# Optimization experiments

Hardware: AMD Instinct MI355X
Metric: run time of the kernel (lower is better)

Reference implementation:

```python
import jax, jax.numpy as jnp
import numpy as np

B, S, D, H = 2, 2048, 1024, 16
HD = D // H           # head_dim = 64
WINDOW = 64           # sparse_block_size (default attention_window)
GLOBAL = 16           # global_tokens


def setup_inputs() -> dict:
    key = jax.random.key(0)
    ks = jax.random.split(key, 12)
    sc = 0.02
    return {
        "query": jax.random.normal(ks[0], (B, S, D), jnp.float32),
        "key":   jax.random.normal(ks[1], (B, S, D), jnp.float32),
        "value": jax.random.normal(ks[2], (B, S, D), jnp.float32),
        "Wq": jax.random.normal(ks[3], (D, D), jnp.float32) * sc,
        "bq": jnp.zeros((D,), jnp.float32),
        "Wk": jax.random.normal(ks[4], (D, D), jnp.float32) * sc,
        "bk": jnp.zeros((D,), jnp.float32),
        "Wv": jax.random.normal(ks[5], (D, D), jnp.float32) * sc,
        "bv": jnp.zeros((D,), jnp.float32),
        "Wo": jax.random.normal(ks[6], (D, D), jnp.float32) * sc,
        "bo": jnp.zeros((D,), jnp.float32),
    }


def _sparse_mask(seq_len, window, n_global):
    # band: j in [i - window//2, i + window//2] inclusive
    idx = jnp.arange(seq_len)
    band = jnp.abs(idx[:, None] - idx[None, :]) <= (window // 2)
    glob = (idx[:, None] < n_global) | (idx[None, :] < n_global)
    return (band | glob)  # [S, S] bool


def reference(query, key, value, Wq, bq, Wk, bk, Wv, bv, Wo, bo):
    # projections (torch Linear: x @ W.T + b), split heads -> [B, H, S, HD]
    def heads(x, W, b):
        return (x @ W.T + b).reshape(B, -1, H, HD).transpose(0, 2, 1, 3)

    q = heads(query, Wq, bq)
    k = heads(key, Wk, bk)
    v = heads(value, Wv, bv)

    scores = jnp.einsum("bhqd,bhkd->bhqk", q, k) / jnp.sqrt(jnp.float32(HD))
    mask = _sparse_mask(S, WINDOW, GLOBAL)  # [S, S]
    scores = jnp.where(mask[None, None, :, :], scores, jnp.float32(-1e9))
    attn = jax.nn.softmax(scores, axis=-1)  # dropout is identity in eval
    ctx = jnp.einsum("bhqk,bhkd->bhqd", attn, v)
    out = ctx.transpose(0, 2, 1, 3).reshape(B, -1, D) @ Wo.T + bo
    return out, attn
```

## Files before the change

kernel.cpp:

```cpp
#include <hip/hip_runtime.h>
#include <hip/hip_bf16.h>
#include <hip/hip_fp16.h>

typedef _Float16 half8 __attribute__((ext_vector_type(8)));
typedef _Float16 half4 __attribute__((ext_vector_type(4)));
typedef float f32x4 __attribute__((ext_vector_type(4)));

#define S_LEN 2048
#define D_MODEL 1024
#define NH 16
#define HEAD_D 64
#define BATCH 2
#define NGLOB 16

__global__ __launch_bounds__(256) void cvt_f32_f16(const float* __restrict__ src,
                                                   _Float16* __restrict__ dst, int n) {
  int i = (blockIdx.x * 256 + threadIdx.x) * 4;
  if (i < n) {
    f32x4 v = *(const f32x4*)(src + i);
    half4 h;
    h[0] = (_Float16)v[0]; h[1] = (_Float16)v[1];
    h[2] = (_Float16)v[2]; h[3] = (_Float16)v[3];
    *(half4*)(dst + i) = h;
  }
}

__device__ __forceinline__ void load_lds16(const void* g, void* l) {
  __builtin_amdgcn_global_load_lds((const __attribute__((address_space(1))) void*)g,
                                   (__attribute__((address_space(3))) void*)l, 16, 0, 0);
}

__global__ __launch_bounds__(256) void gemm_bt_f16(
    const _Float16* __restrict__ A,
    const _Float16* __restrict__ W,
    const float*    __restrict__ bias,
    float*          __restrict__ Cf,
    _Float16*       __restrict__ Ch,
    int M, int N, int K)
{
  __shared__ _Float16 sA[128 * 32];
  __shared__ _Float16 sW[128 * 32];
  const int tid = threadIdx.x;
  const int l = tid & 63;
  const int w = tid >> 6;
  const int wr = w >> 1, wc = w & 1;
  const int m0 = blockIdx.y * 128, n0 = blockIdx.x * 128;

  f32x4 acc[4][4] = {};

  for (int k0 = 0; k0 < K; k0 += 32) {
    {
      int c = tid;
      int row = c >> 2, kc = c & 3;
      load_lds16(A + (size_t)(m0 + row) * K + k0 + kc * 8, sA + c * 8);
      load_lds16(W + (size_t)(n0 + row) * K + k0 + kc * 8, sW + c * 8);
      c = tid + 256;
      row = c >> 2; kc = c & 3;
      load_lds16(A + (size_t)(m0 + row) * K + k0 + kc * 8, sA + c * 8);
      load_lds16(W + (size_t)(n0 + row) * K + k0 + kc * 8, sW + c * 8);
    }
    __syncthreads();

    half8 av[4], bv[4];
#pragma unroll
    for (int mi = 0; mi < 4; ++mi)
      av[mi] = *(const half8*)&sA[(wr * 64 + mi * 16 + (l & 15)) * 32 + (l >> 4) * 8];
#pragma unroll
    for (int ni = 0; ni < 4; ++ni)
      bv[ni] = *(const half8*)&sW[(wc * 64 + ni * 16 + (l & 15)) * 32 + (l >> 4) * 8];
#pragma unroll
    for (int mi = 0; mi < 4; ++mi)
#pragma unroll
      for (int ni = 0; ni < 4; ++ni)
        acc[mi][ni] = __builtin_amdgcn_mfma_f32_16x16x32_f16(av[mi], bv[ni], acc[mi][ni], 0, 0, 0);
    __syncthreads();
  }

#pragma unroll
  for (int mi = 0; mi < 4; ++mi) {
#pragma unroll
    for (int ni = 0; ni < 4; ++ni) {
      int row = m0 + wr * 64 + mi * 16 + ((l >> 4) << 2);
      int col = n0 + wc * 64 + ni * 16 + (l & 15);
      float bc = bias[col];
#pragma unroll
      for (int r = 0; r < 4; ++r) {
        float v = acc[mi][ni][r] + bc;
        size_t idx = (size_t)(row + r) * N + col;
        if (Cf) Cf[idx] = v;
        if (Ch) Ch[idx] = (_Float16)v;
      }
    }
  }
}

__global__ __launch_bounds__(256) void attn_band(
    const _Float16* __restrict__ Qh, const _Float16* __restrict__ Kh,
    const _Float16* __restrict__ Vh,
    float* __restrict__ attn, _Float16* __restrict__ ctx)
{
  __shared__ float Kb[96 * 65];
  __shared__ float Vb[96 * 65];
  __shared__ float Kg[16 * 65];
  __shared__ float Vg[16 * 65];
  __shared__ float qbuf[4][64];
  __shared__ float pbuf[4][128];

  const int bid = blockIdx.x;
  const int rb = bid & 63;
  const int h  = (bid >> 6) & 15;
  const int b  = bid >> 10;
  const int i0 = rb * 32;
  const int jb0 = max(i0 - 32, 0);
  const int jb1 = min(i0 + 63, S_LEN - 1);
  const int Wn = jb1 - jb0 + 1;
  const int tid = threadIdx.x;

  for (int s = tid; s < Wn * 16; s += 256) {
    int j = s >> 4, d4 = (s & 15) << 2;
    size_t base = ((size_t)b * S_LEN + jb0 + j) * D_MODEL + h * HEAD_D + d4;
    half4 kv = *(const half4*)(Kh + base);
    half4 vv = *(const half4*)(Vh + base);
    int o = j * 65 + d4;
    Kb[o] = (float)kv[0]; Kb[o+1] = (float)kv[1]; Kb[o+2] = (float)kv[2]; Kb[o+3] = (float)kv[3];
    Vb[o] = (float)vv[0]; Vb[o+1] = (float)vv[1]; Vb[o+2] = (float)vv[2]; Vb[o+3] = (float)vv[3];
  }
  {
    int s = tid;
    int j = s >> 4, d4 = (s & 15) << 2;
    size_t base = ((size_t)b * S_LEN + j) * D_MODEL + h * HEAD_D + d4;
    half4 kv = *(const half4*)(Kh + base);
    half4 vv = *(const half4*)(Vh + base);
    int o = j * 65 + d4;
    Kg[o] = (float)kv[0]; Kg[o+1] = (float)kv[1]; Kg[o+2] = (float)kv[2]; Kg[o+3] = (float)kv[3];
    Vg[o] = (float)vv[0]; Vg[o+1] = (float)vv[1]; Vg[o+2] = (float)vv[2]; Vg[o+3] = (float)vv[3];
  }
  __syncthreads();

  const int l = tid & 63, w = tid >> 6;
  for (int rr = 0; rr < 8; ++rr) {
    const int i = i0 + w * 8 + rr;
    if (i < NGLOB) continue;

    qbuf[w][l] = (float)Qh[((size_t)b * S_LEN + i) * D_MODEL + h * HEAD_D + l];

    const int b0n = max(i - 32, 16);
    const int b1n = min(i + 32, S_LEN - 1);
    const int nj = 16 + (b1n - b0n + 1);

    const int  j1 = (l < 16) ? l : (b0n + l - 16);
    const bool v1 = l < nj;
    const int  jj2 = l + 64;
    const bool v2 = jj2 < nj;
    const int  j2 = v2 ? (b0n + jj2 - 16) : b0n;

    const float* kr1 = (l < 16) ? &Kg[l * 65] : &Kb[((v1 ? j1 : b0n) - jb0) * 65];
    const float* kr2 = &Kb[(j2 - jb0) * 65];

    float s1 = 0.f, s2 = 0.f;
#pragma unroll 8
    for (int d = 0; d < 64; ++d) {
      float qd = qbuf[w][d];
      s1 += qd * kr1[d];
      s2 += qd * kr2[d];
    }
    s1 *= 0.125f; s2 *= 0.125f;
    if (!v1) s1 = -1e30f;
    if (!v2) s2 = -1e30f;

    float mx = fmaxf(s1, s2);
#pragma unroll
    for (int o = 32; o; o >>= 1) mx = fmaxf(mx, __shfl_xor(mx, o));
    float e1 = v1 ? __expf(s1 - mx) : 0.f;
    float e2 = v2 ? __expf(s2 - mx) : 0.f;
    float sm = e1 + e2;
#pragma unroll
    for (int o = 32; o; o >>= 1) sm += __shfl_xor(sm, o);
    float inv = 1.f / sm;
    float p1 = e1 * inv, p2 = e2 * inv;

    pbuf[w][l] = p1;
    pbuf[w][64 + l] = p2;

    float* arow = attn + ((size_t)(b * NH + h) * S_LEN + i) * S_LEN;
#pragma unroll
    for (int t = 0; t < 8; ++t) {
      const int lo = t * 256;
      const int j0 = lo + l * 4;
      f32x4 o4 = {0.f, 0.f, 0.f, 0.f};
      const bool hasAny = (lo < NGLOB) || !((b1n < lo) || (b0n >= lo + 256));
      if (hasAny) {
#pragma unroll
        for (int r = 0; r < 4; ++r) {
          int j = j0 + r;
          float v = 0.f;
          if (j < NGLOB) v = pbuf[w][j];
          else if (j >= b0n && j <= b1n) v = pbuf[w][16 + j - b0n];
          o4[r] = v;
        }
      }
      *(f32x4*)(arow + j0) = o4;
    }

    float c = 0.f;
    for (int jj = 0; jj < nj; ++jj) {
      float p = pbuf[w][jj];
      const float* vr = (jj < 16) ? &Vg[jj * 65] : &Vb[(b0n + jj - 16 - jb0) * 65];
      c += p * vr[l];
    }
    ctx[((size_t)b * S_LEN + i) * D_MODEL + h * HEAD_D + l] = (_Float16)c;
  }
}

__global__ __launch_bounds__(256) void attn_global(
    const _Float16* __restrict__ Qh, const _Float16* __restrict__ Kh,
    const _Float16* __restrict__ Vh,
    float* __restrict__ attn, _Float16* __restrict__ ctx)
{
  __shared__ float p[S_LEN];
  __shared__ float qbuf[64];
  __shared__ float red[8];
  __shared__ float part[4][64];

  const int bid = blockIdx.x;
  const int i = bid & 15;
  const int h = (bid >> 4) & 15;
  const int b = bid >> 8;
  const int tid = threadIdx.x;

  if (tid < 64) qbuf[tid] = (float)Qh[((size_t)b * S_LEN + i) * D_MODEL + h * HEAD_D + tid];
  __syncthreads();

  float lmax = -1e30f;
  for (int j = tid; j < S_LEN; j += 256) {
    const half8* kr = (const half8*)(Kh + ((size_t)b * S_LEN + j) * D_MODEL + h * HEAD_D);
    float s = 0.f;
#pragma unroll
    for (int c8 = 0; c8 < 8; ++c8) {
      half8 kv = kr[c8];
#pragma unroll
      for (int r = 0; r < 8; ++r) s += qbuf[c8 * 8 + r] * (float)kv[r];
    }
    s *= 0.125f;
    p[j] = s;
    lmax = fmaxf(lmax, s);
  }
#pragma unroll
  for (int o = 32; o; o >>= 1) lmax = fmaxf(lmax, __shfl_xor(lmax, o));
  if ((tid & 63) == 0) red[tid >> 6] = lmax;
  __syncthreads();
  const float mx = fmaxf(fmaxf(red[0], red[1]), fmaxf(red[2], red[3]));

  float lsum = 0.f;
  for (int j = tid; j < S_LEN; j += 256) {
    float e = __expf(p[j] - mx);
    p[j] = e;
    lsum += e;
  }
#pragma unroll
  for (int o = 32; o; o >>= 1) lsum += __shfl_xor(lsum, o);
  if ((tid & 63) == 0) red[4 + (tid >> 6)] = lsum;
  __syncthreads();
  const float inv = 1.f / (red[4] + red[5] + red[6] + red[7]);

  float* arow = attn + ((size_t)(b * NH + h) * S_LEN + i) * S_LEN;
  for (int j = tid; j < S_LEN; j += 256) {
    float pv = p[j] * inv;
    p[j] = pv;
    arow[j] = pv;
  }
  __syncthreads();

  const int d = tid & 63, c4 = tid >> 6;
  float c = 0.f;
  for (int j = c4 * 512; j < c4 * 512 + 512; ++j)
    c += p[j] * (float)Vh[((size_t)b * S_LEN + j) * D_MODEL + h * HEAD_D + d];
  part[c4][d] = c;
  __syncthreads();
  if (tid < 64) {
    float cc = part[0][tid] + part[1][tid] + part[2][tid] + part[3][tid];
    ctx[((size_t)b * S_LEN + i) * D_MODEL + h * HEAD_D + tid] = (_Float16)cc;
  }
}

extern "C" void kernel_launch(void* const* d_in, const int* in_sizes, int n_in,
                              void* d_out, int out_size, void* d_ws, size_t ws_size,
                              hipStream_t stream) {
  const float* query = (const float*)d_in[0];
  const float* key   = (const float*)d_in[1];
  const float* value = (const float*)d_in[2];
  const float* Wq = (const float*)d_in[3];
  const float* bq = (const float*)d_in[4];
  const float* Wk = (const float*)d_in[5];
  const float* bk = (const float*)d_in[6];
  const float* Wv = (const float*)d_in[7];
  const float* bv = (const float*)d_in[8];
  const float* Wo = (const float*)d_in[9];
  const float* bo = (const float*)d_in[10];

  float* out  = (float*)d_out;
  float* attn = out + (size_t)BATCH * S_LEN * D_MODEL;

  const size_t XN = (size_t)BATCH * S_LEN * D_MODEL;
  const size_t WN = (size_t)D_MODEL * D_MODEL;
  _Float16* ws   = (_Float16*)d_ws;
  _Float16* X16  = ws;
  _Float16* W16q = ws + XN;
  _Float16* W16k = W16q + WN;
  _Float16* W16v = W16k + WN;
  _Float16* W16o = W16v + WN;
  _Float16* Q16  = W16o + WN;
  _Float16* K16  = Q16 + XN;
  _Float16* V16  = K16 + XN;
  _Float16* C16  = V16 + XN;

  const int M = BATCH * S_LEN;

  cvt_f32_f16<<<WN / 1024, 256, 0, stream>>>(Wq, W16q, (int)WN);
  cvt_f32_f16<<<WN / 1024, 256, 0, stream>>>(Wk, W16k, (int)WN);
  cvt_f32_f16<<<WN / 1024, 256, 0, stream>>>(Wv, W16v, (int)WN);
  cvt_f32_f16<<<WN / 1024, 256, 0, stream>>>(Wo, W16o, (int)WN);

  dim3 gg(D_MODEL / 128, M / 128);

  cvt_f32_f16<<<XN / 1024, 256, 0, stream>>>(query, X16, (int)XN);
  gemm_bt_f16<<<gg, 256, 0, stream>>>(X16, W16q, bq, nullptr, Q16, M, D_MODEL, D_MODEL);
  cvt_f32_f16<<<XN / 1024, 256, 0, stream>>>(key, X16, (int)XN);
  gemm_bt_f16<<<gg, 256, 0, stream>>>(X16, W16k, bk, nullptr, K16, M, D_MODEL, D_MODEL);
  cvt_f32_f16<<<XN / 1024, 256, 0, stream>>>(value, X16, (int)XN);
  gemm_bt_f16<<<gg, 256, 0, stream>>>(X16, W16v, bv, nullptr, V16, M, D_MODEL, D_MODEL);

  attn_band<<<BATCH * NH * (S_LEN / 32), 256, 0, stream>>>(Q16, K16, V16, attn, C16);
  attn_global<<<BATCH * NH * NGLOB, 256, 0, stream>>>(Q16, K16, V16, attn, C16);

  gemm_bt_f16<<<gg, 256, 0, stream>>>(C16, W16o, bo, out, nullptr, M, D_MODEL, D_MODEL);
}
```

Baseline: 845.5 us.

## Batch QKV projections and conversions into single launches, narrow output GEMM tiles

Merges the three input conversions and four weight conversions into two grid-indexed kernels, and runs the Q/K/V projections as one GEMM launch with a z-dimension selecting the operand set. The output projection now uses a 128x64 tile kernel, which doubles the block count from 256 to 512 and fills more CUs on a 256-CU device. The aim is to cut launch overhead and raise occupancy for the GEMMs. It needs two extra fp16 activation buffers in the workspace, because the inputs no longer share one buffer.

Result: faster. 789.4 us (-6.6%).

```diff
diff --git a/kernel.cpp b/kernel.cpp
--- a/kernel.cpp
+++ b/kernel.cpp
@@ -13,15 +13,35 @@
 #define BATCH 2
 #define NGLOB 16
 
-__global__ __launch_bounds__(256) void cvt_f32_f16(const float* __restrict__ src,
-                                                   _Float16* __restrict__ dst, int n) {
+__global__ __launch_bounds__(256) void cvt_in3(
+    const float* __restrict__ s0, const float* __restrict__ s1, const float* __restrict__ s2,
+    _Float16* __restrict__ d0, _Float16* __restrict__ d1, _Float16* __restrict__ d2, int n) {
+  const float* s = (blockIdx.y == 0) ? s0 : (blockIdx.y == 1) ? s1 : s2;
+  _Float16*   d = (blockIdx.y == 0) ? d0 : (blockIdx.y == 1) ? d1 : d2;
   int i = (blockIdx.x * 256 + threadIdx.x) * 4;
   if (i < n) {
-    f32x4 v = *(const f32x4*)(src + i);
+    f32x4 v = *(const f32x4*)(s + i);
     half4 h;
     h[0] = (_Float16)v[0]; h[1] = (_Float16)v[1];
     h[2] = (_Float16)v[2]; h[3] = (_Float16)v[3];
-    *(half4*)(dst + i) = h;
+    *(half4*)(d + i) = h;
+  }
+}
+
+__global__ __launch_bounds__(256) void cvt_w4(
+    const float* __restrict__ s0, const float* __restrict__ s1,
+    const float* __restrict__ s2, const float* __restrict__ s3,
+    _Float16* __restrict__ d0, _Float16* __restrict__ d1,
+    _Float16* __restrict__ d2, _Float16* __restrict__ d3, int n) {
+  const float* s = (blockIdx.y == 0) ? s0 : (blockIdx.y == 1) ? s1 : (blockIdx.y == 2) ? s2 : s3;
+  _Float16*   d = (blockIdx.y == 0) ? d0 : (blockIdx.y == 1) ? d1 : (blockIdx.y == 2) ? d2 : d3;
+  int i = (blockIdx.x * 256 + threadIdx.x) * 4;
+  if (i < n) {
+    f32x4 v = *(const f32x4*)(s + i);
+    half4 h;
+    h[0] = (_Float16)v[0]; h[1] = (_Float16)v[1];
+    h[2] = (_Float16)v[2]; h[3] = (_Float16)v[3];
+    *(half4*)(d + i) = h;
   }
 }
 
@@ -30,14 +50,19 @@
                                    (__attribute__((address_space(3))) void*)l, 16, 0, 0);
 }
 
-__global__ __launch_bounds__(256) void gemm_bt_f16(
-    const _Float16* __restrict__ A,
-    const _Float16* __restrict__ W,
-    const float*    __restrict__ bias,
-    float*          __restrict__ Cf,
-    _Float16*       __restrict__ Ch,
+__global__ __launch_bounds__(256) void gemm_qkv_f16(
+    const _Float16* __restrict__ A0, const _Float16* __restrict__ A1, const _Float16* __restrict__ A2,
+    const _Float16* __restrict__ W0, const _Float16* __restrict__ W1, const _Float16* __restrict__ W2,
+    const float* __restrict__ b0, const float* __restrict__ b1, const float* __restrict__ b2,
+    _Float16* __restrict__ C0, _Float16* __restrict__ C1, _Float16* __restrict__ C2,
     int M, int N, int K)
 {
+  const int z = blockIdx.z;
+  const _Float16* A = (z == 0) ? A0 : (z == 1) ? A1 : A2;
+  const _Float16* W = (z == 0) ? W0 : (z == 1) ? W1 : W2;
+  const float* bias = (z == 0) ? b0 : (z == 1) ? b1 : b2;
+  _Float16* Ch      = (z == 0) ? C0 : (z == 1) ? C1 : C2;
+
   __shared__ _Float16 sA[128 * 32];
   __shared__ _Float16 sW[128 * 32];
   const int tid = threadIdx.x;
@@ -86,10 +111,66 @@
 #pragma unroll
       for (int r = 0; r < 4; ++r) {
         float v = acc[mi][ni][r] + bc;
-        size_t idx = (size_t)(row + r) * N + col;
-        if (Cf) Cf[idx] = v;
-        if (Ch) Ch[idx] = (_Float16)v;
+        Ch[(size_t)(row + r) * N + col] = (_Float16)v;
       }
+    }
+  }
+}
+
+__global__ __launch_bounds__(256) void gemm_bt64_f16(
+    const _Float16* __restrict__ A,
+    const _Float16* __restrict__ W,
+    const float*    __restrict__ bias,
+    float*          __restrict__ Cf,
+    int M, int N, int K)
+{
+  __shared__ _Float16 sA[128 * 32];
+  __shared__ _Float16 sW[64 * 32];
+  const int tid = threadIdx.x;
+  const int l = tid & 63;
+  const int w = tid >> 6;
+  const int wr = w >> 1, wc = w & 1;
+  const int m0 = blockIdx.y * 128, n0 = blockIdx.x * 64;
+
+  f32x4 acc[4][2] = {};
+
+  for (int k0 = 0; k0 < K; k0 += 32) {
+    {
+      int c = tid;
+      int row = c >> 2, kc = c & 3;
+      load_lds16(A + (size_t)(m0 + row) * K + k0 + kc * 8, sA + c * 8);
+      load_lds16(W + (size_t)(n0 + row) * K + k0 + kc * 8, sW + c * 8);
+      c = tid + 256;
+      row = c >> 2; kc = c & 3;
+      load_lds16(A + (size_t)(m0 + row) * K + k0 + kc * 8, sA + c * 8);
+    }
+    __syncthreads();
+
+    half8 av[4], bv[2];
+#pragma unroll
+    for (int mi = 0; mi < 4; ++mi)
+      av[mi] = *(const half8*)&sA[(wr * 64 + mi * 16 + (l & 15)) * 32 + (l >> 4) * 8];
+#pragma unroll
+    for (int ni = 0; ni < 2; ++ni)
+      bv[ni] = *(const half8*)&sW[(wc * 32 + ni * 16 + (l & 15)) * 32 + (l >> 4) * 8];
+#pragma unroll
+    for (int mi = 0; mi < 4; ++mi)
+#pragma unroll
+      for (int ni = 0; ni < 2; ++ni)
+        acc[mi][ni] = __builtin_amdgcn_mfma_f32_16x16x32_f16(av[mi], bv[ni], acc[mi][ni], 0, 0, 0);
+    __syncthreads();
+  }
+
+#pragma unroll
+  for (int mi = 0; mi < 4; ++mi) {
+#pragma unroll
+    for (int ni = 0; ni < 2; ++ni) {
+      int row = m0 + wr * 64 + mi * 16 + ((l >> 4) << 2);
+      int col = n0 + wc * 32 + ni * 16 + (l & 15);
+      float bc = bias[col];
+#pragma unroll
+      for (int r = 0; r < 4; ++r)
+        Cf[(size_t)(row + r) * N + col] = acc[mi][ni][r] + bc;
     }
   }
 }
@@ -304,8 +385,10 @@
   const size_t XN = (size_t)BATCH * S_LEN * D_MODEL;
   const size_t WN = (size_t)D_MODEL * D_MODEL;
   _Float16* ws   = (_Float16*)d_ws;
-  _Float16* X16  = ws;
-  _Float16* W16q = ws + XN;
+  _Float16* X16q = ws;
+  _Float16* X16k = X16q + XN;
+  _Float16* X16v = X16k + XN;
+  _Float16* W16q = X16v + XN;
   _Float16* W16k = W16q + WN;
   _Float16* W16v = W16k + WN;
   _Float16* W16o = W16v + WN;
@@ -316,22 +399,18 @@
 
   const int M = BATCH * S_LEN;
 
-  cvt_f32_f16<<<WN / 1024, 256, 0, stream>>>(Wq, W16q, (int)WN);
-  cvt_f32_f16<<<WN / 1024, 256, 0, stream>>>(Wk, W16k, (int)WN);
-  cvt_f32_f16<<<WN / 1024, 256, 0, stream>>>(Wv, W16v, (int)WN);
-  cvt_f32_f16<<<WN / 1024, 256, 0, stream>>>(Wo, W16o, (int)WN);
-
-  dim3 gg(D_MODEL / 128, M / 128);
-
-  cvt_f32_f16<<<XN / 1024, 256, 0, stream>>>(query, X16, (int)XN);
-  gemm_bt_f16<<<gg, 256, 0, stream>>>(X16, W16q, bq, nullptr, Q16, M, D_MODEL, D_MODEL);
-  cvt_f32_f16<<<XN / 1024, 256, 0, stream>>>(key, X16, (int)XN);
-  gemm_bt_f16<<<gg, 256, 0, stream>>>(X16, W16k, bk, nullptr, K16, M, D_MODEL, D_MODEL);
-  cvt_f32_f16<<<XN / 1024, 256, 0, stream>>>(value, X16, (int)XN);
-  gemm_bt_f16<<<gg, 256, 0, stream>>>(X16, W16v, bv, nullptr, V16, M, D_MODEL, D_MODEL);
+  dim3 gi(XN / 1024, 3);
+  cvt_in3<<<gi, 256, 0, stream>>>(query, key, value, X16q, X16k, X16v, (int)XN);
+  dim3 gw(WN / 1024, 4);
+  cvt_w4<<<gw, 256, 0, stream>>>(Wq, Wk, Wv, Wo, W16q, W16k, W16v, W16o, (int)WN);
+
+  dim3 gp(D_MODEL / 128, M / 128, 3);
+  gemm_qkv_f16<<<gp, 256, 0, stream>>>(X16q, X16k, X16v, W16q, W16k, W16v,
+                                       bq, bk, bv, Q16, K16, V16, M, D_MODEL, D_MODEL);
 
   attn_band<<<BATCH * NH * (S_LEN / 32), 256, 0, stream>>>(Q16, K16, V16, attn, C16);
   attn_global<<<BATCH * NH * NGLOB, 256, 0, stream>>>(Q16, K16, V16, attn, C16);
 
-  gemm_bt_f16<<<gg, 256, 0, stream>>>(C16, W16o, bo, out, nullptr, M, D_MODEL, D_MODEL);
-}
+  dim3 gf(D_MODEL / 64, M / 128);
+  gemm_bt64_f16<<<gf, 256, 0, stream>>>(C16, W16o, bo, out, M, D_MODEL, D_MODEL);
+}
```
